# Performance work log

Hardware: AMD Instinct MI355X
Metric: run time of the kernel (lower is better)

The kernel has to match this reference:

```python
import jax, jax.numpy as jnp
import numpy as np

K, M_EMB, N_HID, D_CTX, D_ATT, M_COV = 128, 256, 256, 684, 512, 256
B, H, W = 64, 16, 48


def gru_cell(x, h, W_ih, W_hh, b_ih, b_hh):
    # PyTorch GRUCell semantics
    gi = x @ W_ih.T + b_ih
    gh = h @ W_hh.T + b_hh
    i_r, i_z, i_n = jnp.split(gi, 3, axis=-1)
    h_r, h_z, h_n = jnp.split(gh, 3, axis=-1)
    r = jax.nn.sigmoid(i_r + h_r)
    z = jax.nn.sigmoid(i_z + h_z)
    n = jnp.tanh(i_n + r * h_n)
    return (1.0 - z) * n + z * h


def setup_inputs() -> dict:
    key = jax.random.key(0)
    ks = jax.random.split(key, 24)
    s = 0.02
    inp = {
        'y': jax.random.randint(ks[0], (B,), 0, K),
        'y_mask': jnp.ones((B,), jnp.float32),
        'context': jax.random.normal(ks[1], (B, D_CTX, H, W), jnp.float32),
        'pre_hidden': jax.random.normal(ks[2], (B, N_HID), jnp.float32),
        'alpha_past': jax.random.uniform(ks[3], (B, H, W), jnp.float32),
        'emb': jax.random.normal(ks[4], (K + 1, M_EMB)) * s,
        'W_ih1': jax.random.normal(ks[5], (3 * N_HID, M_EMB)) * s,
        'W_hh1': jax.random.normal(ks[6], (3 * N_HID, N_HID)) * s,
        'b_ih1': jnp.zeros((3 * N_HID,)),
        'b_hh1': jnp.zeros((3 * N_HID,)),
        'conv_Ua_w': jax.random.normal(ks[7], (D_ATT, D_CTX, 1, 1)) * s,
        'conv_Ua_b': jnp.zeros((D_ATT,)),
        'Wa': jax.random.normal(ks[8], (D_ATT, N_HID)) * s,
        'conv_Q_w': jax.random.normal(ks[9], (M_COV, 1, 3, 3)) * s,
        'Uf': jax.random.normal(ks[10], (D_ATT, M_COV)) * s,
        'Uf_b': jnp.zeros((D_ATT,)),
        'va': jax.random.normal(ks[11], (1, D_ATT)) * s,
        'va_b': jnp.zeros((1,)),
        'W_ih2': jax.random.normal(ks[12], (3 * N_HID, D_CTX)) * s,
        'W_hh2': jax.random.normal(ks[13], (3 * N_HID, N_HID)) * s,
        'b_ih2': jnp.zeros((3 * N_HID,)),
        'b_hh2': jnp.zeros((3 * N_HID,)),
        'Wct': jax.random.normal(ks[14], (M_EMB, D_CTX)) * s,
        'Wct_b': jnp.zeros((M_EMB,)),
        'Wht': jax.random.normal(ks[15], (M_EMB, N_HID)) * s,
        'Wht_b': jnp.zeros((M_EMB,)),
        'W0': jax.random.normal(ks[16], (K, M_EMB // 2)) * s,
        'W0_b': jnp.zeros((K,)),
    }
    return inp


def reference(y, y_mask, context, pre_hidden, alpha_past, emb,
              W_ih1, W_hh1, b_ih1, b_hh1, conv_Ua_w, conv_Ua_b, Wa,
              conv_Q_w, Uf, Uf_b, va, va_b,
              W_ih2, W_hh2, b_ih2, b_hh2, Wct, Wct_b, Wht, Wht_b, W0, W0_b):
    embedded = emb[y]                                           # [B, m]
    s_hat = gru_cell(embedded, pre_hidden, W_ih1, W_hh1, b_ih1, b_hh1)
    s_hat = y_mask[:, None] * s_hat + (1.0 - y_mask)[:, None] * pre_hidden

    Wa_h1 = s_hat @ Wa.T                                        # [B, A]
    # 1x1 conv == channel projection, output in NHWC layout
    Ua_ctx = jnp.einsum('bdhw,ad->bhwa', context, conv_Ua_w[:, :, 0, 0]) + conv_Ua_b
    # 3x3 coverage conv over past attention map
    cover_F = jax.lax.conv_general_dilated(
        alpha_past[:, None, :, :], conv_Q_w, (1, 1), 'SAME',
        dimension_numbers=('NCHW', 'OIHW', 'NCHW'))              # [B, M, H, W]
    cover_F = jnp.transpose(cover_F, (0, 2, 3, 1))               # [B, H, W, M]
    cover_vector = cover_F @ Uf.T + Uf_b                         # [B, H, W, A]

    e_att = jnp.tanh(Ua_ctx + Wa_h1[:, None, None, :] + cover_vector)
    alpha = (e_att @ va.T + va_b)[..., 0].reshape(e_att.shape[0], -1)  # [B, H*W]
    alpha = jax.nn.softmax(alpha, axis=1)

    ct = jnp.einsum('bdp,bp->bd', context.reshape(context.shape[0], context.shape[1], -1), alpha)

    s = gru_cell(ct, s_hat, W_ih2, W_hh2, b_ih2, b_hh2)
    s = y_mask[:, None] * s + (1.0 - y_mask)[:, None] * s_hat

    logit = ct @ Wct.T + Wct_b + s @ Wht.T + Wht_b + embedded    # [B, m]
    logit = logit.reshape(logit.shape[0], -1, 2).max(axis=2)     # maxout -> [B, m/2]
    out = logit @ W0.T + W0_b                                    # [B, K]
    return out, s, alpha.reshape(alpha.shape[0], H, W)
```

## Files before the change

### kernel.cpp

```cpp
#include <hip/hip_runtime.h>
#include <hip/hip_bf16.h>
#include <math.h>

#define BB 64
#define KV 128
#define ME 256
#define NH 256
#define DC 684
#define DA 512
#define MC 256
#define HH_ 16
#define WW_ 48
#define HW_ 768
#define NS 22

typedef __attribute__((ext_vector_type(8))) short bf16x8;
typedef __attribute__((ext_vector_type(4))) float f32x4;

#define WS_G     0
#define WS_RB    (WS_G + 4608)
#define WS_EMB   (WS_RB + 32768)
#define WS_SH    (WS_EMB + 16384)
#define WS_AL    (WS_SH + 16384)
#define WS_CT    (WS_AL + 49152)
#define WS_APACK (WS_CT + 43776)
#define WS_GI    (WS_APACK + 180224)
#define WS_GH    (WS_GI + 49152)
#define WS_LG    WS_GI
#define WS_BP    (WS_GH + 49152)
#define WS_AL2   (WS_BP + 17301504)
#define NEED_BYTES ((size_t)(441600 + 17301504 + 49152) * 4)

static __device__ __forceinline__ unsigned short f2b(float v) {
    __hip_bfloat16 h = __float2bfloat16(v);
    return *reinterpret_cast<unsigned short*>(&h);
}

template <int AUX>
static __device__ __forceinline__ void gl_lds16(const unsigned short* g,
                                                unsigned short* l) {
    __builtin_amdgcn_global_load_lds(
        (const __attribute__((address_space(1))) unsigned int*)g,
        (__attribute__((address_space(3))) unsigned int*)l, 16, 0, AUX);
}

__global__ __launch_bounds__(512) void k_prep(
    const float* __restrict__ ctx, const float* __restrict__ Ua,
    const float* __restrict__ Uf, const float* __restrict__ convQ,
    const int* __restrict__ y, const float* __restrict__ emb,
    unsigned short* __restrict__ Bpack, unsigned short* __restrict__ Apack,
    float* __restrict__ G, float* __restrict__ embedded) {
    __shared__ unsigned short Ts[64 * 360];
    int bx = blockIdx.x, t = threadIdx.x;
    if (bx < 768) {
        int b = bx / 12, pt = bx % 12, p0 = pt * 64;
        int w = t >> 6, p = t & 63;
        unsigned short* dst = Bpack + (long)(b * 12 + pt) * 22 * 2048;
        for (int ch = 0; ch < 2; ch++) {
            int dbase = ch * 352;
            if (ch) __syncthreads();
#pragma unroll
            for (int iter = 0; iter < 11; iter++) {
                int d0 = dbase + iter * 32 + w * 4;
                float v0 = 0.f, v1 = 0.f, v2 = 0.f, v3 = 0.f;
                const float* src = ctx + ((long)b * DC + d0) * HW_ + p0 + p;
                if (d0 + 0 < DC) v0 = src[0];
                if (d0 + 1 < DC) v1 = src[HW_];
                if (d0 + 2 < DC) v2 = src[2 * HW_];
                if (d0 + 3 < DC) v3 = src[3 * HW_];
                unsigned u01 = (unsigned)f2b(v0) | ((unsigned)f2b(v1) << 16);
                unsigned u23 = (unsigned)f2b(v2) | ((unsigned)f2b(v3) << 16);
                *(uint2*)&Ts[p * 360 + (d0 - dbase)] = make_uint2(u01, u23);
            }
            __syncthreads();
            int so = t >> 8;
            int tt = t & 255;
            int pp = tt >> 2, slot = tt & 3;
#pragma unroll
            for (int s2 = 0; s2 < 12; s2 += 2) {
                int sl = s2 + so;
                if (sl < 11) {
                    int s = ch * 11 + sl;
                    bf16x8 v = *(const bf16x8*)&Ts[pp * 360 + sl * 32 +
                                                   ((slot ^ ((pp >> 1) & 3))
                                                    << 3)];
                    *(bf16x8*)(dst + (long)(s * 256 + tt) * 8) = v;
                }
            }
        }
    } else if (bx < 856) {
        int bi = bx - 768;
#pragma unroll
        for (int r = 0; r < 8; r++) {
            int idx = bi * 4096 + r * 512 + t;
            int e = idx & 7, slot = (idx >> 3) & 3;
            int a = (idx >> 5) & 511, s = idx >> 14;
            int d = s * 32 + ((slot ^ ((a >> 1) & 3)) << 3) + e;
            float v = (d < DC) ? Ua[a * DC + d] : 0.f;
            Apack[idx] = f2b(v);
        }
    } else if (bx < 865) {
        int idx = (bx - 856) * 512 + t;
        if (idx < DA * 9) {
            int a = idx / 9, k = idx % 9;
            float s = 0.f;
            for (int m = 0; m < MC; m++) s += Uf[a * MC + m] * convQ[m * 9 + k];
            G[idx] = s;
        }
    } else {
        int b = bx - 865;
        if (t < ME) embedded[b * ME + t] = emb[y[b] * ME + t];
    }
}

__global__ __launch_bounds__(256) void k_G(const float* __restrict__ Uf,
                                           const float* __restrict__ convQ,
                                           float* __restrict__ G) {
    int idx = blockIdx.x * 256 + threadIdx.x;
    if (idx >= DA * 9) return;
    int a = idx / 9, k = idx % 9;
    float s = 0.f;
    for (int m = 0; m < MC; m++) s += Uf[a * MC + m] * convQ[m * 9 + k];
    G[idx] = s;
}

__global__ __launch_bounds__(256) void k_prepA(const float* __restrict__ Ua,
                                               unsigned short* __restrict__ Apack) {
    int idx = blockIdx.x * 256 + threadIdx.x;
    if (idx >= NS * DA * 32) return;
    int e = idx & 7, slot = (idx >> 3) & 3;
    int a = (idx >> 5) & 511, s = idx >> 14;
    int d = s * 32 + ((slot ^ ((a >> 1) & 3)) << 3) + e;
    float v = (d < DC) ? Ua[a * DC + d] : 0.f;
    Apack[idx] = f2b(v);
}

__global__ __launch_bounds__(256) void k_emb(const int* __restrict__ y,
                                             const float* __restrict__ emb,
                                             float* __restrict__ embedded) {
    int b = blockIdx.x, t = threadIdx.x;
    embedded[b * ME + t] = emb[y[b] * ME + t];
}

__global__ __launch_bounds__(256) void k_rows256(
    const float* __restrict__ X, const float* __restrict__ W,
    const float* __restrict__ bias, const float* __restrict__ bias2,
    float* __restrict__ out, int outStride) {
    __shared__ float Xs[64 * 257];
    __shared__ float Ws[4 * 260];
    int t = threadIdx.x, w = t >> 6, lane = t & 63;
    for (int i = t; i < 64 * 256; i += 256) {
        int bb = i >> 8, k = i & 255;
        Xs[bb * 257 + k] = X[bb * 256 + k];
    }
    int r = blockIdx.x * 4 + w;
    *(f32x4*)(Ws + w * 260 + lane * 4) = *(const f32x4*)(W + r * 256 + lane * 4);
    __syncthreads();
    const float* xrow = Xs + lane * 257;
    const float* wrow = Ws + w * 260;
    float acc = 0.f;
#pragma unroll 8
    for (int k = 0; k < 256; k++) acc += wrow[k] * xrow[k];
    acc += bias[r];
    if (bias2) acc += bias2[r];
    out[lane * outStride + r] = acc;
}

__global__ __launch_bounds__(256) void k_gih1(
    const float* __restrict__ embedded, const float* __restrict__ pre_hidden,
    const float* __restrict__ W_ih1, const float* __restrict__ W_hh1,
    const float* __restrict__ b_ih1, const float* __restrict__ b_hh1,
    float* __restrict__ gi, float* __restrict__ gh) {
    __shared__ float Xs[64 * 257];
    __shared__ float Ws[4 * 260];
    int bx = blockIdx.x, t = threadIdx.x, w = t >> 6, lane = t & 63;
    const float *X, *W, *bias;
    float* outp;
    int r;
    if (bx < 192) {
        X = embedded; W = W_ih1; bias = b_ih1; outp = gi; r = bx * 4 + w;
    } else {
        X = pre_hidden; W = W_hh1; bias = b_hh1; outp = gh; r = (bx - 192) * 4 + w;
    }
    for (int i = t; i < 64 * 256; i += 256) {
        int bb = i >> 8, k = i & 255;
        Xs[bb * 257 + k] = X[bb * 256 + k];
    }
    *(f32x4*)(Ws + w * 260 + lane * 4) = *(const f32x4*)(W + r * 256 + lane * 4);
    __syncthreads();
    const float* xrow = Xs + lane * 257;
    const float* wrow = Ws + w * 260;
    float acc = 0.f;
#pragma unroll 8
    for (int k = 0; k < 256; k++) acc += wrow[k] * xrow[k];
    outp[lane * 768 + r] = acc + bias[r];
}

__global__ __launch_bounds__(256) void k_gih2(
    const float* __restrict__ ctv, const float* __restrict__ s_hat,
    const float* __restrict__ W_ih2, const float* __restrict__ W_hh2,
    const float* __restrict__ b_ih2, const float* __restrict__ b_hh2,
    float* __restrict__ gi, float* __restrict__ gh) {
    __shared__ float Xs[64 * 257];
    __shared__ float Ws[4 * 260];
    int bx = blockIdx.x, t = threadIdx.x, w = t >> 6, lane = t & 63;
    if (bx < 192) {
        int r = bx * 4 + w;
        float acc = 0.f;
        for (int c = 0; c < 3; c++) {
            int c0 = c * 228;
            __syncthreads();
            for (int i = t; i < 64 * 228; i += 256) {
                int bb = i / 228, kk = i - bb * 228;
                Xs[bb * 229 + kk] = ctv[bb * DC + c0 + kk];
            }
            for (int j = lane; j < 228; j += 64)
                Ws[w * 260 + j] = W_ih2[r * DC + c0 + j];
            __syncthreads();
            const float* xrow = Xs + lane * 229;
            const float* wrow = Ws + w * 260;
#pragma unroll 4
            for (int k = 0; k < 228; k++) acc += wrow[k] * xrow[k];
        }
        gi[lane * 768 + r] = acc + b_ih2[r];
    } else {
        int r = (bx - 192) * 4 + w;
        for (int i = t; i < 64 * 256; i += 256) {
            int bb = i >> 8, k = i & 255;
            Xs[bb * 257 + k] = s_hat[bb * 256 + k];
        }
        *(f32x4*)(Ws + w * 260 + lane * 4) =
            *(const f32x4*)(W_hh2 + r * 256 + lane * 4);
        __syncthreads();
        const float* xrow = Xs + lane * 257;
        const float* wrow = Ws + w * 260;
        float acc = 0.f;
#pragma unroll 8
        for (int k = 0; k < 256; k++) acc += wrow[k] * xrow[k];
        gh[lane * 768 + r] = acc + b_hh2[r];
    }
}

__global__ __launch_bounds__(256) void k_gru(const float* __restrict__ gi,
                                             const float* __restrict__ gh,
                                             const float* __restrict__ h,
                                             const float* __restrict__ y_mask,
                                             float* __restrict__ outp) {
    int b = blockIdx.x, t = threadIdx.x;
    float hv = h[b * NH + t];
    float r = 1.f / (1.f + expf(-(gi[b * 768 + t] + gh[b * 768 + t])));
    float z = 1.f / (1.f + expf(-(gi[b * 768 + 256 + t] + gh[b * 768 + 256 + t])));
    float n = tanhf(gi[b * 768 + 512 + t] + r * gh[b * 768 + 512 + t]);
    float sv = (1.f - z) * n + z * hv;
    float m = y_mask[b];
    outp[b * NH + t] = m * sv + (1.f - m) * hv;
}

__global__ __launch_bounds__(512, 1) void k_att3(
    const unsigned short* __restrict__ Apack,
    const unsigned short* __restrict__ Bpack, const float* __restrict__ G,
    const float* __restrict__ rb, const float* __restrict__ va,
    const float* __restrict__ apast, float* __restrict__ alogit0,
    float* __restrict__ alogit1) {
    __shared__ __attribute__((aligned(16))) unsigned short lsA[2][8192];
    __shared__ __attribute__((aligned(16))) unsigned short lsB[2][6144];
    __shared__ float ap_s[18 * 50];
    __shared__ float part_s[8][96];
    int pt = blockIdx.x, ah = blockIdx.y, b = blockIdx.z;
    int t = threadIdx.x, w = t >> 6, lane = t & 63;
    int l15 = lane & 15, lg = lane >> 4;
    int aw = w & 3, pw = w >> 2;
    int sx = lg ^ ((l15 >> 1) & 3);

    for (int idx = t; idx < 900; idx += 512) {
        int hh = idx / 50, ww = idx % 50;
        float v = 0.f;
        if (hh >= 1 && hh <= HH_ && ww >= 1 && ww <= WW_)
            v = apast[b * HW_ + (hh - 1) * WW_ + (ww - 1)];
        ap_s[idx] = v;
    }
    __syncthreads();

    const unsigned short* Ap0 = Apack + ah * 8192 + w * 1024 + lane * 8;
    const unsigned short* Bp0[2];
    int ldst[2];
    {
#pragma unroll
        for (int i = 0; i < 2; i++) {
            int l = w * 2 + i;
            if (l >= 12) l -= 12;
            int c = l >> 2, q = l & 3;
            Bp0[i] = Bpack + (long)(b * 12 + pt * 3 + c) * 22 * 2048 + q * 512 +
                     lane * 8;
            ldst[i] = c * 2048 + q * 512;
        }
    }

#define STAGE(S, BUF)                                                        \
    do {                                                                     \
        _Pragma("unroll") for (int i_ = 0; i_ < 2; i_++)                     \
            gl_lds16<0>(Ap0 + (long)(S)*16384 + i_ * 512,                    \
                        &lsA[BUF][w * 1024 + i_ * 512]);                     \
        _Pragma("unroll") for (int i_ = 0; i_ < 2; i_++)                     \
            gl_lds16<2>(Bp0[i_] + (long)(S)*2048, &lsB[BUF][ldst[i_]]);      \
    } while (0)

#define STEP_BODY(CUR)                                                       \
    do {                                                                     \
        bf16x8 af[4], bf[6];                                                 \
        _Pragma("unroll") for (int i = 0; i < 4; i++)                        \
            af[i] = *(const bf16x8*)&lsA[CUR][(aw * 64 + i * 16 + l15) * 32 +\
                                             sx * 8];                        \
        _Pragma("unroll") for (int j = 0; j < 6; j++)                        \
            bf[j] = *(const bf16x8*)&lsB[CUR][(pw * 96 + j * 16 + l15) * 32 +\
                                             sx * 8];                        \
        _Pragma("unroll") for (int i = 0; i < 4; i++)                        \
            _Pragma("unroll") for (int j = 0; j < 6; j++)                    \
                acc[i][j] = __builtin_amdgcn_mfma_f32_16x16x32_bf16(         \
                    af[i], bf[j], acc[i][j], 0, 0, 0);                       \
    } while (0)

    f32x4 acc[4][6];
#pragma unroll
    for (int i = 0; i < 4; i++)
#pragma unroll
        for (int j = 0; j < 6; j++) acc[i][j] = {0.f, 0.f, 0.f, 0.f};

    STAGE(0, 0);
    STAGE(1, 1);

    for (int s = 0; s < NS - 1; s++) {
        int cur = s & 1;
        asm volatile("s_waitcnt vmcnt(4)" ::: "memory");
        __builtin_amdgcn_sched_barrier(0);
        __builtin_amdgcn_s_barrier();
        __builtin_amdgcn_sched_barrier(0);
        STEP_BODY(cur);
        __builtin_amdgcn_s_barrier();
        __builtin_amdgcn_sched_barrier(0);
        if (s + 2 < NS) STAGE(s + 2, cur);
    }
    asm volatile("s_waitcnt vmcnt(0)" ::: "memory");
    __builtin_amdgcn_sched_barrier(0);
    __builtin_amdgcn_s_barrier();
    __builtin_amdgcn_sched_barrier(0);
    STEP_BODY((NS - 1) & 1);
#undef STAGE
#undef STEP_BODY

    float partial[6] = {0.f, 0.f, 0.f, 0.f, 0.f, 0.f};
#pragma unroll
    for (int i = 0; i < 4; i++) {
#pragma unroll
        for (int r = 0; r < 4; r++) {
            int a = ah * 256 + aw * 64 + i * 16 + lg * 4 + r;
            float rbv = rb[b * DA + a];
            float vav = va[a];
            const float* Ga = G + a * 9;
            float g0 = Ga[0], g1 = Ga[1], g2 = Ga[2], g3 = Ga[3], g4 = Ga[4];
            float g5 = Ga[5], g6 = Ga[6], g7 = Ga[7], g8 = Ga[8];
#pragma unroll
            for (int j = 0; j < 6; j++) {
                int p = pt * 192 + pw * 96 + j * 16 + l15;
                int hh = p / WW_, ww = p % WW_;
                const float* ap = ap_s + hh * 50 + ww;
                float cov = g0 * ap[0] + g1 * ap[1] + g2 * ap[2] +
                            g3 * ap[50] + g4 * ap[51] + g5 * ap[52] +
                            g6 * ap[100] + g7 * ap[101] + g8 * ap[102];
                float e = tanhf(acc[i][j][r] + rbv + cov);
                partial[j] += vav * e;
            }
        }
    }
#pragma unroll
    for (int j = 0; j < 6; j++) {
        partial[j] += __shfl_xor(partial[j], 16);
        partial[j] += __shfl_xor(partial[j], 32);
    }
    if (lane < 16) {
#pragma unroll
        for (int j = 0; j < 6; j++) part_s[w][j * 16 + lane] = partial[j];
    }
    __syncthreads();
    if (t < 192) {
        int pg = t / 96, pl = t % 96;
        float sum = part_s[pg * 4 + 0][pl] + part_s[pg * 4 + 1][pl] +
                    part_s[pg * 4 + 2][pl] + part_s[pg * 4 + 3][pl];
        float* dst = ah ? alogit1 : alogit0;
        dst[b * HW_ + pt * 192 + t] = sum;
    }
}

#define LDW 40
__global__ __launch_bounds__(256) void k_att_lds(
    const unsigned short* __restrict__ Apack, const float* __restrict__ ctx,
    const float* __restrict__ G, const float* __restrict__ rb,
    const float* __restrict__ va, const float* __restrict__ apast,
    float* __restrict__ alogit) {
    __shared__ __attribute__((aligned(16))) short lsB[2][64 * LDW];
    __shared__ float ap_s[18 * 50];
    __shared__ float part_s[4 * 64];
    int b = blockIdx.y;
    int p0 = blockIdx.x * 64;
    int t = threadIdx.x;
    int w = t >> 6, lane = t & 63;
    int l15 = lane & 15, lg = lane >> 4;
    int sxA = lg ^ ((l15 >> 1) & 3);
    int pq = t & 15, kp = t >> 4;
    const float* ctx_b = ctx + (long)b * DC * HW_ + p0;

    for (int idx = t; idx < 900; idx += 256) {
        int hh = idx / 50, ww = idx % 50;
        float v = 0.f;
        if (hh >= 1 && hh <= HH_ && ww >= 1 && ww <= WW_)
            v = apast[b * HW_ + (hh - 1) * WW_ + (ww - 1)];
        ap_s[idx] = v;
    }

#define CTXLOAD(FA, FB, S)                                                   \
    do {                                                                     \
        int d_ = (S) * 32 + 2 * kp;                                          \
        const float* s0_ = ctx_b + (long)d_ * HW_ + pq;                      \
        bool g0_ = d_ < DC, g1_ = (d_ + 1) < DC;                             \
        _Pragma("unroll") for (int j_ = 0; j_ < 4; j_++) {                   \
            FA[j_] = g0_ ? s0_[16 * j_] : 0.f;                               \
            FB[j_] = g1_ ? s0_[HW_ + 16 * j_] : 0.f;                         \
        }                                                                    \
    } while (0)
#define STAGEW(FA, FB, BUF)                                                  \
    do {                                                                     \
        _Pragma("unroll") for (int j_ = 0; j_ < 4; j_++) {                   \
            ((unsigned*)lsB[BUF])[(pq + 16 * j_) * (LDW / 2) + kp] =         \
                (unsigned)f2b(FA[j_]) | ((unsigned)f2b(FB[j_]) << 16);       \
        }                                                                    \
    } while (0)
#define ALOAD(AF, S)                                                         \
    do {                                                                     \
        _Pragma("unroll") for (int i_ = 0; i_ < 8; i_++)                     \
            AF[i_] = *(const bf16x8*)(Apack +                                \
                ((long)((S)*512 + w * 128 + i_ * 16 + l15) * 4 + sxA) * 8);  \
    } while (0)
#define BREAD(BF, BUF)                                                       \
    do {                                                                     \
        _Pragma("unroll") for (int j_ = 0; j_ < 4; j_++)                     \
            BF[j_] = *(const bf16x8*)(&lsB[BUF][(j_ * 16 + l15) * LDW +      \
                                               lg * 8]);                     \
    } while (0)
#define MFMA8x4(AF, BF)                                                      \
    do {                                                                     \
        _Pragma("unroll") for (int i_ = 0; i_ < 8; i_++)                     \
            _Pragma("unroll") for (int j_ = 0; j_ < 4; j_++)                 \
                acc[i_][j_] = __builtin_amdgcn_mfma_f32_16x16x32_bf16(       \
                    AF[i_], BF[j_], acc[i_][j_], 0, 0, 0);                   \
    } while (0)

    f32x4 acc[8][4];
#pragma unroll
    for (int i = 0; i < 8; i++)
#pragma unroll
        for (int j = 0; j < 4; j++) acc[i][j] = {0.f, 0.f, 0.f, 0.f};

    float fa0[4], fb0[4], fa1[4], fb1[4];
    bf16x8 afr0[8], afr1[8], bfr[4];

    CTXLOAD(fa1, fb1, 0);
    ALOAD(afr0, 0);
    STAGEW(fa1, fb1, 0);
    CTXLOAD(fa1, fb1, 1);
    __syncthreads();

    for (int ss = 0; ss < NS; ss += 2) {
        if (ss + 2 < NS) CTXLOAD(fa0, fb0, ss + 2);
        ALOAD(afr1, ss + 1);
        BREAD(bfr, 0);
        STAGEW(fa1, fb1, 1);
        MFMA8x4(afr0, bfr);
        __syncthreads();
        if (ss + 3 < NS) CTXLOAD(fa1, fb1, ss + 3);
        if (ss + 2 < NS) {
            ALOAD(afr0, ss + 2);
            BREAD(bfr, 1);
            STAGEW(fa0, fb0, 0);
            MFMA8x4(afr1, bfr);
        } else {
            BREAD(bfr, 1);
            MFMA8x4(afr1, bfr);
        }
        __syncthreads();
    }

    float partial[4] = {0.f, 0.f, 0.f, 0.f};
#pragma unroll
    for (int i = 0; i < 8; i++) {
#pragma unroll
        for (int r = 0; r < 4; r++) {
            int a = w * 128 + i * 16 + lg * 4 + r;
            float rbv = rb[b * DA + a];
            float vav = va[a];
            const float* Ga = G + a * 9;
            float g0 = Ga[0], g1 = Ga[1], g2 = Ga[2], g3 = Ga[3], g4 = Ga[4];
            float g5 = Ga[5], g6 = Ga[6], g7 = Ga[7], g8 = Ga[8];
#pragma unroll
            for (int j = 0; j < 4; j++) {
                int p = p0 + j * 16 + l15;
                int hh = p / WW_, ww = p % WW_;
                const float* ap = ap_s + hh * 50 + ww;
                float cov = g0 * ap[0] + g1 * ap[1] + g2 * ap[2] +
                            g3 * ap[50] + g4 * ap[51] + g5 * ap[52] +
                            g6 * ap[100] + g7 * ap[101] + g8 * ap[102];
                float e = tanhf(acc[i][j][r] + rbv + cov);
                partial[j] += vav * e;
            }
        }
    }
#pragma unroll
    for (int j = 0; j < 4; j++) {
        partial[j] += __shfl_xor(partial[j], 16);
        partial[j] += __shfl_xor(partial[j], 32);
    }
    if (lane < 16) {
#pragma unroll
        for (int j = 0; j < 4; j++) part_s[w * 64 + j * 16 + lane] = partial[j];
    }
    __syncthreads();
    if (t < 64) {
        float s = part_s[t] + part_s[64 + t] + part_s[128 + t] +
                  part_s[192 + t];
        alogit[b * HW_ + p0 + t] = s;
    }
}

__global__ __launch_bounds__(256) void k_ctsm(const float* __restrict__ ctx,
                                              const float* __restrict__ alogit0,
                                              const float* __restrict__ alogit1,
                                              float* __restrict__ ct,
                                              float* __restrict__ alpha_out) {
    __shared__ float al_s[HW_];
    __shared__ float red[16];
    int b = blockIdx.y, t = threadIdx.x;
    float v[3];
    float mx = -1e30f;
    for (int i = 0; i < 3; i++) {
        int idx = b * HW_ + i * 256 + t;
        v[i] = alogit0[idx] + alogit1[idx];
        mx = fmaxf(mx, v[i]);
    }
    for (int off = 32; off > 0; off >>= 1) mx = fmaxf(mx, __shfl_down(mx, off));
    if ((t & 63) == 0) red[t >> 6] = mx;
    __syncthreads();
    if (t == 0) red[0] = fmaxf(fmaxf(red[0], red[1]), fmaxf(red[2], red[3]));
    __syncthreads();
    mx = red[0];
    float sum = 0.f;
    for (int i = 0; i < 3; i++) {
        v[i] = expf(v[i] - mx);
        sum += v[i];
    }
    for (int off = 32; off > 0; off >>= 1) sum += __shfl_down(sum, off);
    if ((t & 63) == 0) red[8 + (t >> 6)] = sum;
    __syncthreads();
    if (t == 0) red[8] = red[8] + red[9] + red[10] + red[11];
    __syncthreads();
    float inv = 1.f / red[8];
    for (int i = 0; i < 3; i++) {
        float a = v[i] * inv;
        al_s[i * 256 + t] = a;
        if (blockIdx.x == 0) alpha_out[b * HW_ + i * 256 + t] = a;
    }
    __syncthreads();
    int dc0 = blockIdx.x * 114;
    int wave = t >> 6, lane = t & 63;
    for (int d = dc0 + wave; d < dc0 + 114; d += 4) {
        const float* row = &ctx[((long)b * DC + d) * HW_];
        float s = 0.f;
#pragma unroll
        for (int q = 0; q < 12; q++) s += row[lane + q * 64] * al_s[lane + q * 64];
        for (int off = 32; off > 0; off >>= 1) s += __shfl_down(s, off);
        if (lane == 0) ct[b * DC + d] = s;
    }
}

__global__ __launch_bounds__(256) void k_logit(
    const float* __restrict__ ctv, const float* __restrict__ s,
    const float* __restrict__ embedded, const float* __restrict__ Wct,
    const float* __restrict__ Wht, const float* __restrict__ Wct_b,
    const float* __restrict__ Wht_b, float* __restrict__ lg) {
    __shared__ float Xs[64 * 257];
    __shared__ float Ws[4 * 232];
    int t = threadIdx.x, w = t >> 6, lane = t & 63;
    int r = blockIdx.x * 4 + w;
    float acc = 0.f;
    for (int c = 0; c < 3; c++) {
        int c0 = c * 228;
        __syncthreads();
        for (int i = t; i < 64 * 228; i += 256) {
            int bb = i / 228, kk = i - bb * 228;
            Xs[bb * 229 + kk] = ctv[bb * DC + c0 + kk];
        }
        for (int j = lane; j < 228; j += 64) Ws[w * 232 + j] = Wct[r * DC + c0 + j];
        __syncthreads();
        const float* xrow = Xs + lane * 229;
        const float* wrow = Ws + w * 232;
#pragma unroll 4
        for (int k = 0; k < 228; k++) acc += wrow[k] * xrow[k];
    }
    __syncthreads();
    for (int i = t; i < 64 * 256; i += 256) {
        int bb = i >> 8, k = i & 255;
        Xs[bb * 257 + k] = s[bb * 256 + k];
    }
    __syncthreads();
    const float* xrow2 = Xs + lane * 257;
    const float* wr = Wht + r * 256;
    float acc2 = 0.f;
#pragma unroll 8
    for (int k = 0; k < 256; k++) acc2 += wr[k] * xrow2[k];
    lg[lane * 256 + r] = acc + acc2 + Wct_b[r] + Wht_b[r] + embedded[lane * 256 + r];
}

__global__ __launch_bounds__(256) void k_head(const float* __restrict__ lg,
                                              const float* __restrict__ W0,
                                              const float* __restrict__ W0_b,
                                              float* __restrict__ out) {
    __shared__ float Xs[64 * 129];
    __shared__ float Ws[4 * 132];
    int t = threadIdx.x, w = t >> 6, lane = t & 63;
    for (int i = t; i < 64 * 128; i += 256) {
        int bb = i >> 7, m = i & 127;
        Xs[bb * 129 + m] = fmaxf(lg[bb * 256 + 2 * m], lg[bb * 256 + 2 * m + 1]);
    }
    int r = blockIdx.x * 4 + w;
    Ws[w * 132 + lane] = W0[r * 128 + lane];
    Ws[w * 132 + 64 + lane] = W0[r * 128 + 64 + lane];
    __syncthreads();
    const float* xrow = Xs + lane * 129;
    const float* wrow = Ws + w * 132;
    float acc = 0.f;
#pragma unroll 8
    for (int k = 0; k < 128; k++) acc += wrow[k] * xrow[k];
    out[lane * KV + r] = acc + W0_b[r];
}

extern "C" void kernel_launch(void* const* d_in, const int* in_sizes, int n_in,
                              void* d_out, int out_size, void* d_ws,
                              size_t ws_size, hipStream_t stream) {
    const int* y = (const int*)d_in[0];
    const float* y_mask = (const float*)d_in[1];
    const float* context = (const float*)d_in[2];
    const float* pre_hidden = (const float*)d_in[3];
    const float* alpha_past = (const float*)d_in[4];
    const float* emb = (const float*)d_in[5];
    const float* W_ih1 = (const float*)d_in[6];
    const float* W_hh1 = (const float*)d_in[7];
    const float* b_ih1 = (const float*)d_in[8];
    const float* b_hh1 = (const float*)d_in[9];
    const float* conv_Ua_w = (const float*)d_in[10];
    const float* conv_Ua_b = (const float*)d_in[11];
    const float* Wa = (const float*)d_in[12];
    const float* conv_Q_w = (const float*)d_in[13];
    const float* Uf = (const float*)d_in[14];
    const float* Uf_b = (const float*)d_in[15];
    const float* va = (const float*)d_in[16];
    const float* va_b = (const float*)d_in[17];
    const float* W_ih2 = (const float*)d_in[18];
    const float* W_hh2 = (const float*)d_in[19];
    const float* b_ih2 = (const float*)d_in[20];
    const float* b_hh2 = (const float*)d_in[21];
    const float* Wct = (const float*)d_in[22];
    const float* Wct_b = (const float*)d_in[23];
    const float* Wht = (const float*)d_in[24];
    const float* Wht_b = (const float*)d_in[25];
    const float* W0 = (const float*)d_in[26];
    const float* W0_b = (const float*)d_in[27];

    float* ws = (float*)d_ws;
    float* out = (float*)d_out;
    float* G = ws + WS_G;
    float* rbias = ws + WS_RB;
    float* embedded = ws + WS_EMB;
    float* s_hat = ws + WS_SH;
    float* alogit = ws + WS_AL;
    float* ctv = ws + WS_CT;
    unsigned short* Apack = (unsigned short*)(ws + WS_APACK);
    float* gi = ws + WS_GI;
    float* gh = ws + WS_GH;
    float* lg = ws + WS_LG;
    unsigned short* Bpack = (unsigned short*)(ws + WS_BP);
    float* alogit2 = ws + WS_AL2;
    float* s_out = out + 8192;
    float* alpha_out = out + 24576;

    bool fast = ws_size >= NEED_BYTES;

    if (fast) {
        k_prep<<<dim3(929), dim3(512), 0, stream>>>(context, conv_Ua_w, Uf,
                                                    conv_Q_w, y, emb, Bpack,
                                                    Apack, G, embedded);
    } else {
        k_G<<<dim3(18), dim3(256), 0, stream>>>(Uf, conv_Q_w, G);
        k_prepA<<<dim3((NS * DA * 32 + 255) / 256), dim3(256), 0, stream>>>(
            conv_Ua_w, Apack);
        k_emb<<<dim3(64), dim3(256), 0, stream>>>(y, emb, embedded);
        hipMemsetAsync(alogit2, 0, 49152 * sizeof(float), stream);
    }
    k_gih1<<<dim3(384), dim3(256), 0, stream>>>(embedded, pre_hidden, W_ih1,
                                                W_hh1, b_ih1, b_hh1, gi, gh);
    k_gru<<<dim3(64), dim3(256), 0, stream>>>(gi, gh, pre_hidden, y_mask, s_hat);
    k_rows256<<<dim3(128), dim3(256), 0, stream>>>(s_hat, Wa, conv_Ua_b, Uf_b,
                                                   rbias, 512);
    if (fast) {
        k_att3<<<dim3(4, 2, 64), dim3(512), 0, stream>>>(
            Apack, Bpack, G, rbias, va, alpha_past, alogit, alogit2);
    } else {
        k_att_lds<<<dim3(12, 64), dim3(256), 0, stream>>>(
            Apack, context, G, rbias, va, alpha_past, alogit);
    }
    k_ctsm<<<dim3(6, 64), dim3(256), 0, stream>>>(context, alogit, alogit2,
                                                  ctv, alpha_out);
    k_gih2<<<dim3(384), dim3(256), 0, stream>>>(ctv, s_hat, W_ih2, W_hh2, b_ih2,
                                                b_hh2, gi, gh);
    k_gru<<<dim3(64), dim3(256), 0, stream>>>(gi, gh, s_hat, y_mask, s_out);
    k_logit<<<dim3(64), dim3(256), 0, stream>>>(ctv, s_out, embedded, Wct, Wht,
                                                Wct_b, Wht_b, lg);
    k_head<<<dim3(32), dim3(256), 0, stream>>>(lg, W0, W0_b, out);
}
```

Before: 256.0 us.

## Split attention GEMM into four 128-wide A-slices with 256-thread blocks

The attention-logit kernel moves from 512-thread blocks covering 256 attention dims to 256-thread blocks covering 128 dims, with a grid of 4x4x64 instead of 4x2x64. Partial logits from the four slices go to a quad workspace and are summed in the softmax kernel. The intent is more blocks and higher occupancy, since the launch bound no longer forces one block per CU. The cost is that each block reloads the same context B tile, so B-side global traffic doubles.

```diff
diff --git a/kernel.cpp b/kernel.cpp
--- a/kernel.cpp
+++ b/kernel.cpp
@@ -28,8 +28,8 @@
 #define WS_GH    (WS_GI + 49152)
 #define WS_LG    WS_GI
 #define WS_BP    (WS_GH + 49152)
-#define WS_AL2   (WS_BP + 17301504)
-#define NEED_BYTES ((size_t)(441600 + 17301504 + 49152) * 4)
+#define WS_ALQ   (WS_BP + 17301504)
+#define NEED_BYTES ((size_t)(441600 + 17301504 + 196608) * 4)
 
 static __device__ __forceinline__ unsigned short f2b(float v) {
     __hip_bfloat16 h = __float2bfloat16(v);
@@ -256,23 +256,22 @@
     outp[b * NH + t] = m * sv + (1.f - m) * hv;
 }
 
-__global__ __launch_bounds__(512, 1) void k_att3(
+__global__ __launch_bounds__(256) void k_att3(
     const unsigned short* __restrict__ Apack,
     const unsigned short* __restrict__ Bpack, const float* __restrict__ G,
     const float* __restrict__ rb, const float* __restrict__ va,
-    const float* __restrict__ apast, float* __restrict__ alogit0,
-    float* __restrict__ alogit1) {
-    __shared__ __attribute__((aligned(16))) unsigned short lsA[2][8192];
+    const float* __restrict__ apast, float* __restrict__ alq) {
+    __shared__ __attribute__((aligned(16))) unsigned short lsA[2][4096];
     __shared__ __attribute__((aligned(16))) unsigned short lsB[2][6144];
     __shared__ float ap_s[18 * 50];
-    __shared__ float part_s[8][96];
+    __shared__ float part_s[4][96];
     int pt = blockIdx.x, ah = blockIdx.y, b = blockIdx.z;
     int t = threadIdx.x, w = t >> 6, lane = t & 63;
     int l15 = lane & 15, lg = lane >> 4;
-    int aw = w & 3, pw = w >> 2;
+    int aw = w & 1, pw = w >> 1;
     int sx = lg ^ ((l15 >> 1) & 3);
 
-    for (int idx = t; idx < 900; idx += 512) {
+    for (int idx = t; idx < 900; idx += 256) {
         int hh = idx / 50, ww = idx % 50;
         float v = 0.f;
         if (hh >= 1 && hh <= HH_ && ww >= 1 && ww <= WW_)
@@ -281,19 +280,16 @@
     }
     __syncthreads();
 
-    const unsigned short* Ap0 = Apack + ah * 8192 + w * 1024 + lane * 8;
-    const unsigned short* Bp0[2];
-    int ldst[2];
-    {
-#pragma unroll
-        for (int i = 0; i < 2; i++) {
-            int l = w * 2 + i;
-            if (l >= 12) l -= 12;
-            int c = l >> 2, q = l & 3;
-            Bp0[i] = Bpack + (long)(b * 12 + pt * 3 + c) * 22 * 2048 + q * 512 +
-                     lane * 8;
-            ldst[i] = c * 2048 + q * 512;
-        }
+    const unsigned short* Ap0 = Apack + ah * 4096 + w * 1024 + lane * 8;
+    const unsigned short* Bp0[3];
+    int ldst[3];
+#pragma unroll
+    for (int i = 0; i < 3; i++) {
+        int l = w * 3 + i;
+        int c = l >> 2, q = l & 3;
+        Bp0[i] = Bpack + (long)(b * 12 + pt * 3 + c) * 22 * 2048 + q * 512 +
+                 lane * 8;
+        ldst[i] = l * 512;
     }
 
 #define STAGE(S, BUF)                                                        \
@@ -301,7 +297,7 @@
         _Pragma("unroll") for (int i_ = 0; i_ < 2; i_++)                     \
             gl_lds16<0>(Ap0 + (long)(S)*16384 + i_ * 512,                    \
                         &lsA[BUF][w * 1024 + i_ * 512]);                     \
-        _Pragma("unroll") for (int i_ = 0; i_ < 2; i_++)                     \
+        _Pragma("unroll") for (int i_ = 0; i_ < 3; i_++)                     \
             gl_lds16<2>(Bp0[i_] + (long)(S)*2048, &lsB[BUF][ldst[i_]]);      \
     } while (0)
 
@@ -331,7 +327,7 @@
 
     for (int s = 0; s < NS - 1; s++) {
         int cur = s & 1;
-        asm volatile("s_waitcnt vmcnt(4)" ::: "memory");
+        asm volatile("s_waitcnt vmcnt(5)" ::: "memory");
         __builtin_amdgcn_sched_barrier(0);
         __builtin_amdgcn_s_barrier();
         __builtin_amdgcn_sched_barrier(0);
@@ -353,7 +349,7 @@
     for (int i = 0; i < 4; i++) {
 #pragma unroll
         for (int r = 0; r < 4; r++) {
-            int a = ah * 256 + aw * 64 + i * 16 + lg * 4 + r;
+            int a = ah * 128 + aw * 64 + i * 16 + lg * 4 + r;
             float rbv = rb[b * DA + a];
             float vav = va[a];
             const float* Ga = G + a * 9;
@@ -384,10 +380,8 @@
     __syncthreads();
     if (t < 192) {
         int pg = t / 96, pl = t % 96;
-        float sum = part_s[pg * 4 + 0][pl] + part_s[pg * 4 + 1][pl] +
-                    part_s[pg * 4 + 2][pl] + part_s[pg * 4 + 3][pl];
-        float* dst = ah ? alogit1 : alogit0;
-        dst[b * HW_ + pt * 192 + t] = sum;
+        float sum = part_s[2 * pg][pl] + part_s[2 * pg + 1][pl];
+        alq[ah * 49152 + b * HW_ + pt * 192 + t] = sum;
     }
 }
 
@@ -531,8 +525,7 @@
 }
 
 __global__ __launch_bounds__(256) void k_ctsm(const float* __restrict__ ctx,
-                                              const float* __restrict__ alogit0,
-                                              const float* __restrict__ alogit1,
+                                              const float* __restrict__ alq,
                                               float* __restrict__ ct,
                                               float* __restrict__ alpha_out) {
     __shared__ float al_s[HW_];
@@ -542,7 +535,8 @@
     float mx = -1e30f;
     for (int i = 0; i < 3; i++) {
         int idx = b * HW_ + i * 256 + t;
-        v[i] = alogit0[idx] + alogit1[idx];
+        v[i] = (alq[idx] + alq[49152 + idx]) +
+               (alq[98304 + idx] + alq[147456 + idx]);
         mx = fmaxf(mx, v[i]);
     }
     for (int off = 32; off > 0; off >>= 1) mx = fmaxf(mx, __shfl_down(mx, off));
@@ -679,14 +673,13 @@
     float* rbias = ws + WS_RB;
     float* embedded = ws + WS_EMB;
     float* s_hat = ws + WS_SH;
-    float* alogit = ws + WS_AL;
     float* ctv = ws + WS_CT;
     unsigned short* Apack = (unsigned short*)(ws + WS_APACK);
     float* gi = ws + WS_GI;
     float* gh = ws + WS_GH;
     float* lg = ws + WS_LG;
     unsigned short* Bpack = (unsigned short*)(ws + WS_BP);
-    float* alogit2 = ws + WS_AL2;
+    float* alq = ws + WS_ALQ;
     float* s_out = out + 8192;
     float* alpha_out = out + 24576;
 
@@ -701,7 +694,6 @@
         k_prepA<<<dim3((NS * DA * 32 + 255) / 256), dim3(256), 0, stream>>>(
             conv_Ua_w, Apack);
         k_emb<<<dim3(64), dim3(256), 0, stream>>>(y, emb, embedded);
-        hipMemsetAsync(alogit2, 0, 49152 * sizeof(float), stream);
     }
     k_gih1<<<dim3(384), dim3(256), 0, stream>>>(embedded, pre_hidden, W_ih1,
                                                 W_hh1, b_ih1, b_hh1, gi, gh);
@@ -709,14 +701,15 @@
     k_rows256<<<dim3(128), dim3(256), 0, stream>>>(s_hat, Wa, conv_Ua_b, Uf_b,
                                                    rbias, 512);
     if (fast) {
-        k_att3<<<dim3(4, 2, 64), dim3(512), 0, stream>>>(
-            Apack, Bpack, G, rbias, va, alpha_past, alogit, alogit2);
+        k_att3<<<dim3(4, 4, 64), dim3(256), 0, stream>>>(
+            Apack, Bpack, G, rbias, va, alpha_past, alq);
     } else {
+        hipMemsetAsync(alq + 49152, 0, (size_t)3 * 49152 * sizeof(float),
+                       stream);
         k_att_lds<<<dim3(12, 64), dim3(256), 0, stream>>>(
-            Apack, context, G, rbias, va, alpha_past, alogit);
-    }
-    k_ctsm<<<dim3(6, 64), dim3(256), 0, stream>>>(context, alogit, alogit2,
-                                                  ctv, alpha_out);
+            Apack, context, G, rbias, va, alpha_past, alq);
+    }
+    k_ctsm<<<dim3(6, 64), dim3(256), 0, stream>>>(context, alq, ctv, alpha_out);
     k_gih2<<<dim3(384), dim3(256), 0, stream>>>(ctv, s_hat, W_ih2, W_hh2, b_ih2,
                                                 b_hh2, gi, gh);
     k_gru<<<dim3(64), dim3(256), 0, stream>>>(gi, gh, s_hat, y_mask, s_out);
```

After: 304.4 us. +18.9%, slower.
